# Performance work log

Hardware: AMD Instinct MI355X
Metric: run time of the kernel (lower is better)

The kernel has to match this reference:

```python
import jax, jax.numpy as jnp
import numpy as np

N_HEAD = 16
ROPE_BASE = 10000.0


def _rope_tables(T, head_dim, dtype=jnp.float32):
    inv_freq = 1.0 / (ROPE_BASE ** (jnp.arange(0, head_dim, 2, dtype=jnp.float32) / head_dim))
    t = jnp.arange(T, dtype=jnp.float32)
    freqs = t[:, None] * inv_freq[None, :]          # [T, D/2]
    emb = jnp.concatenate([freqs, freqs], axis=-1)  # [T, D]
    return jnp.cos(emb).astype(dtype), jnp.sin(emb).astype(dtype)


def _rotate_half(x):
    d = x.shape[-1] // 2
    return jnp.concatenate([-x[..., d:], x[..., :d]], axis=-1)


def setup_inputs() -> dict:
    key = jax.random.key(0)
    ks = jax.random.split(key, 5)
    B, T, C = 2, 2048, 2048
    s = 1.0 / np.sqrt(C)
    return {
        "x": jax.random.normal(ks[0], (B, T, C), dtype=jnp.float32),
        "wq": jax.random.normal(ks[1], (C, C), dtype=jnp.float32) * s,
        "wk": jax.random.normal(ks[2], (C, C), dtype=jnp.float32) * s,
        "wv": jax.random.normal(ks[3], (C, C), dtype=jnp.float32) * s,
        "wo": jax.random.normal(ks[4], (C, C), dtype=jnp.float32) * s,
    }


def reference(x, wq, wk, wv, wo):
    B, T, C = x.shape
    H = N_HEAD
    D = C // H

    def heads(y):  # [B,T,C] -> [B,H,T,D]
        return y.reshape(B, T, H, D).transpose(0, 2, 1, 3)

    q = heads(x @ wq)
    k = heads(x @ wk)
    v = heads(x @ wv)

    cos, sin = _rope_tables(T, D, x.dtype)          # [T, D]
    cos = cos[None, None, :, :]
    sin = sin[None, None, :, :]
    q = q * cos + _rotate_half(q) * sin
    k = k * cos + _rotate_half(k) * sin

    scale = 1.0 / np.sqrt(D)
    scores = jnp.einsum('bhqd,bhkd->bhqk', q, k) * scale   # [B,H,T,T]
    causal = jnp.tril(jnp.ones((T, T), dtype=bool))
    scores = jnp.where(causal[None, None, :, :], scores, jnp.finfo(scores.dtype).min)
    attn = jax.nn.softmax(scores, axis=-1)
    y = jnp.einsum('bhqk,bhkd->bhqd', attn, v)             # [B,H,T,D]
    y = y.transpose(0, 2, 1, 3).reshape(B, T, C)
    return y @ wo
```

## Files before the change

kernel.cpp:

```cpp
#include <hip/hip_runtime.h>
#include <hip/hip_bf16.h>
#include <math.h>


#define TT 2048
#define CCn 2048
#define HH 16
#define DD 128
#define BBa 2
#define MMr 4096

typedef __attribute__((ext_vector_type(8))) short s16x8;
typedef __attribute__((ext_vector_type(4))) short s16x4;
typedef __attribute__((ext_vector_type(4))) float f32x4;

__device__ __forceinline__ short bf16_of(float f) {
  unsigned u = __float_as_uint(f);
  unsigned r = u + 0x7fffu + ((u >> 16) & 1u);
  return (short)(r >> 16);
}

__device__ __forceinline__ float ex2(float x) {
#if __has_builtin(__builtin_amdgcn_exp2f)
  return __builtin_amdgcn_exp2f(x);
#else
  return exp2f(x);
#endif
}

__device__ __forceinline__ void lds_load16(const void* g, void* l) {
  __builtin_amdgcn_global_load_lds((__attribute__((address_space(1))) void*)g,
                                   (__attribute__((address_space(3))) void*)l,
                                   16, 0, 0);
}

__global__ __launch_bounds__(256) void k_tables(float* __restrict__ cosT,
                                                float* __restrict__ sinT) {
  int idx = blockIdx.x * 256 + threadIdx.x;
  int t = idx >> 6, i = idx & 63;
  float inv = powf(10000.0f, -(float)i * (1.0f / 64.0f));
  float f = (float)t * inv;
  cosT[idx] = cosf(f);
  sinT[idx] = sinf(f);
}

__global__ __launch_bounds__(256) void k_cast_x(const float* __restrict__ x,
                                                short* __restrict__ xb) {
  int i = blockIdx.x * 256 + threadIdx.x;
  f32x4 v = ((const f32x4*)x)[i];
  s16x4 o;
#pragma unroll
  for (int j = 0; j < 4; ++j) o[j] = bf16_of(v[j]);
  ((s16x4*)xb)[i] = o;
}

__global__ __launch_bounds__(256) void k_wtrans(const float* __restrict__ w,
                                                short* __restrict__ wt) {
  __shared__ float tile[32][33];
  int n0 = blockIdx.x * 32, k0 = blockIdx.y * 32;
  int tx = threadIdx.x & 31, ty = threadIdx.x >> 5;
#pragma unroll
  for (int j = 0; j < 4; ++j) {
    int k = ty * 4 + j;
    tile[k][tx] = w[(size_t)(k0 + k) * CCn + n0 + tx];
  }
  __syncthreads();
#pragma unroll
  for (int j = 0; j < 4; ++j) {
    int n = ty * 4 + j;
    wt[(size_t)(n0 + n) * CCn + k0 + tx] = bf16_of(tile[tx][n]);
  }
}

__global__ __launch_bounds__(256) void k_vtrans(const float* __restrict__ src,
                                                short* __restrict__ dst) {
  __shared__ float tile[32][33];
  int bh = blockIdx.y, b = bh >> 4, h = bh & 15;
  int dt = blockIdx.x & 3, tt = blockIdx.x >> 2;
  int tx = threadIdx.x & 31, ty = threadIdx.x >> 5;
  const float* sp = src + ((size_t)(b * TT + tt * 32)) * CCn + h * DD + dt * 32;
#pragma unroll
  for (int j = 0; j < 4; ++j) {
    int tr = ty * 4 + j;
    tile[tr][tx] = sp[(size_t)tr * CCn + tx];
  }
  __syncthreads();
  short* dp = dst + ((size_t)(bh * DD + dt * 32)) * TT + tt * 32;
#pragma unroll
  for (int j = 0; j < 4; ++j) {
    int dr = ty * 4 + j;
    dp[(size_t)dr * TT + tx] = bf16_of(tile[tx][dr]);
  }
}

__global__ __launch_bounds__(256) void k_rope(const float* __restrict__ src,
                                              const float* __restrict__ cosT,
                                              const float* __restrict__ sinT,
                                              short* __restrict__ dst, float mul) {
  int idx = blockIdx.x * 256 + threadIdx.x;
  int i = idx & 63;
  int h = (idx >> 6) & 15;
  int t = (idx >> 10) & 2047;
  int b = idx >> 21;
  const float* row = src + ((size_t)(b * TT + t)) * CCn + h * DD;
  float q0 = row[i], q1 = row[i + 64];
  float c = cosT[t * 64 + i], s = sinT[t * 64 + i];
  short* orow = dst + ((size_t)((b * HH + h) * TT + t)) * DD;
  orow[i] = bf16_of((q0 * c - q1 * s) * mul);
  orow[i + 64] = bf16_of((q1 * c + q0 * s) * mul);
}

#define BKG 64
__global__ __launch_bounds__(256) void k_gemm(const short* __restrict__ A,
                                              const short* __restrict__ Bt,
                                              float* __restrict__ Cc,
                                              int M, int N, int K) {
  __shared__ short As[128 * BKG];
  __shared__ short Bs[128 * BKG];
  const int tid = threadIdx.x, wid = tid >> 6, lane = tid & 63;
  const int wm = wid >> 1, wn = wid & 1;
  const int lr = lane & 15, lk = lane >> 4;
  const int m0 = blockIdx.y * 128, n0 = blockIdx.x * 128;

  f32x4 acc[4][4] = {};
  const int nk = K / BKG;
  for (int kt = 0; kt < nk; ++kt) {
#pragma unroll
    for (int it = 0; it < 4; ++it) {
      int ch = it * 256 + tid;
      int r = ch >> 3, c = (ch & 7) * 8;
      lds_load16(A + (size_t)(m0 + r) * K + kt * BKG + c,
                 As + (size_t)(it * 256 + wid * 64) * 8);
      lds_load16(Bt + (size_t)(n0 + r) * K + kt * BKG + c,
                 Bs + (size_t)(it * 256 + wid * 64) * 8);
    }
    __syncthreads();
#pragma unroll
    for (int ks = 0; ks < 2; ++ks) {
      s16x8 af[4], bf[4];
#pragma unroll
      for (int i = 0; i < 4; ++i) {
        int ar = wm * 64 + i * 16 + lr;
        af[i] = *(const s16x8*)(As + ar * BKG + ks * 32 + lk * 8);
        int br = wn * 64 + i * 16 + lr;
        bf[i] = *(const s16x8*)(Bs + br * BKG + ks * 32 + lk * 8);
      }
#pragma unroll
      for (int i = 0; i < 4; ++i)
#pragma unroll
        for (int j = 0; j < 4; ++j)
          acc[i][j] = __builtin_amdgcn_mfma_f32_16x16x32_bf16(af[i], bf[j],
                                                              acc[i][j], 0, 0, 0);
    }
    __syncthreads();
  }
#pragma unroll
  for (int i = 0; i < 4; ++i)
#pragma unroll
    for (int j = 0; j < 4; ++j) {
      int col = n0 + wn * 64 + j * 16 + lr;
      int rb = m0 + wm * 64 + i * 16 + lk * 4;
#pragma unroll
      for (int r = 0; r < 4; ++r)
        Cc[(size_t)(rb + r) * N + col] = acc[i][j][r];
    }
}

__global__ __launch_bounds__(256) void k_attn(const short* __restrict__ Qb,
                                              const short* __restrict__ Kb,
                                              const short* __restrict__ Vt,
                                              short* __restrict__ yb) {
  __shared__ short Ks[2][64 * 128];
  __shared__ short Vs[128 * 64];
  __shared__ short Ps[4][16 * 72];
  const int tid = threadIdx.x, wid = tid >> 6, lane = tid & 63;
  const int lr = lane & 15, lk = lane >> 4;
  const int bh = blockIdx.y, bx = blockIdx.x;
  const size_t baseQK = (size_t)bh * TT * DD;
  const int b = bh >> 4, h = bh & 15;

  auto stageK = [&](int bi, int kt2) {
#pragma unroll
    for (int it = 0; it < 4; ++it) {
      int ch = it * 256 + tid;
      int r = ch >> 4, cc = ch & 15;
      int cs = cc ^ (r & 7);
      lds_load16(Kb + baseQK + (size_t)(kt2 * 64 + r) * DD + cs * 8,
                 &Ks[bi][(size_t)(it * 256 + wid * 64) * 8]);
    }
  };
  auto stageV = [&](int kt2) {
#pragma unroll
    for (int it = 0; it < 4; ++it) {
      int ch = it * 256 + tid;
      int d = ch >> 3, kc = ch & 7;
      int cs = kc ^ (d & 7);
      lds_load16(Vt + baseQK + (size_t)d * TT + kt2 * 64 + cs * 8,
                 &Vs[(size_t)(it * 256 + wid * 64) * 8]);
    }
  };

#pragma unroll 1
  for (int pass = 0; pass < 2; ++pass) {
    const int qt = pass ? (31 - bx) : bx;
    const int q0 = qt * 64;
    const int qg = q0 + wid * 16 + lr;
    s16x8 qf[4];
#pragma unroll
    for (int ds = 0; ds < 4; ++ds)
      qf[ds] = *(const s16x8*)(Qb + baseQK + (size_t)qg * DD + (ds * 4 + lk) * 8);

    float mrun = -3.0e38f, lrun = 0.f;
    f32x4 yacc[8] = {};

    const int nkt = qt + 1;
    stageK(0, 0);
    stageV(0);
    __syncthreads();
    int buf = 0;
#pragma unroll 1
    for (int kt = 0; kt < nkt; ++kt) {
      if (kt + 1 < nkt) stageK(buf ^ 1, kt + 1);
      f32x4 sf[4] = {};
#pragma unroll
      for (int sub = 0; sub < 4; ++sub) {
        int kr = sub * 16 + lr;
#pragma unroll
        for (int ds = 0; ds < 4; ++ds) {
          int cc = (ds * 4 + lk) ^ (kr & 7);
          s16x8 kf = *(const s16x8*)(&Ks[buf][kr * 128 + cc * 8]);
          sf[sub] = __builtin_amdgcn_mfma_f32_16x16x32_bf16(kf, qf[ds], sf[sub], 0, 0, 0);
        }
      }
      const int kvbase = kt * 64;
      if (kvbase + 63 > q0 + wid * 16) {
#pragma unroll
        for (int sub = 0; sub < 4; ++sub)
#pragma unroll
          for (int r = 0; r < 4; ++r) {
            int kv = kvbase + sub * 16 + lk * 4 + r;
            if (kv > qg) sf[sub][r] = -3.0e38f;
          }
      }
      float tmax = -3.0e38f;
#pragma unroll
      for (int sub = 0; sub < 4; ++sub)
#pragma unroll
        for (int r = 0; r < 4; ++r) tmax = fmaxf(tmax, sf[sub][r]);
      tmax = fmaxf(tmax, __shfl_xor(tmax, 16, 64));
      tmax = fmaxf(tmax, __shfl_xor(tmax, 32, 64));
      if (!__all(tmax <= mrun + 11.0f)) {
        float mnew = fmaxf(mrun, tmax);
        float alpha = ex2(mrun - mnew);
        mrun = mnew;
        lrun *= alpha;
        float ar[4];
#pragma unroll
        for (int r = 0; r < 4; ++r) ar[r] = __shfl(alpha, lk * 4 + r, 64);
#pragma unroll
        for (int dn = 0; dn < 8; ++dn)
#pragma unroll
          for (int r = 0; r < 4; ++r) yacc[dn][r] *= ar[r];
      }
      float psum = 0.f;
#pragma unroll
      for (int sub = 0; sub < 4; ++sub) {
        s16x4 pq;
#pragma unroll
        for (int r = 0; r < 4; ++r) {
          float p = ex2(sf[sub][r] - mrun);
          psum += p;
          pq[r] = bf16_of(p);
        }
        *(s16x4*)(&Ps[wid][lr * 72 + sub * 16 + lk * 4]) = pq;
      }
      psum += __shfl_xor(psum, 16, 64);
      psum += __shfl_xor(psum, 32, 64);
      lrun += psum;
      __syncthreads();
      s16x8 pf0 = *(const s16x8*)(&Ps[wid][lr * 72 + lk * 8]);
      s16x8 pf1 = *(const s16x8*)(&Ps[wid][lr * 72 + 32 + lk * 8]);
#pragma unroll
      for (int dn = 0; dn < 8; ++dn) {
        int d = dn * 16 + lr;
        s16x8 vf0 = *(const s16x8*)(&Vs[d * 64 + (lk ^ (d & 7)) * 8]);
        yacc[dn] = __builtin_amdgcn_mfma_f32_16x16x32_bf16(pf0, vf0, yacc[dn], 0, 0, 0);
        s16x8 vf1 = *(const s16x8*)(&Vs[d * 64 + ((4 + lk) ^ (d & 7)) * 8]);
        yacc[dn] = __builtin_amdgcn_mfma_f32_16x16x32_bf16(pf1, vf1, yacc[dn], 0, 0, 0);
      }
      __syncthreads();
      if (kt + 1 < nkt) stageV(kt + 1);
      buf ^= 1;
    }
    float linv = 1.f / lrun;
    float lr4[4];
#pragma unroll
    for (int r = 0; r < 4; ++r) lr4[r] = __shfl(linv, lk * 4 + r, 64);
#pragma unroll
    for (int dn = 0; dn < 8; ++dn)
#pragma unroll
      for (int r = 0; r < 4; ++r) {
        int t = q0 + wid * 16 + lk * 4 + r;
        int c = h * DD + dn * 16 + lr;
        yb[((size_t)(b * TT + t)) * CCn + c] = bf16_of(yacc[dn][r] * lr4[r]);
      }
  }
}

extern "C" void kernel_launch(void* const* d_in, const int* in_sizes, int n_in,
                              void* d_out, int out_size, void* d_ws, size_t ws_size,
                              hipStream_t stream) {
  const float* x = (const float*)d_in[0];
  const float* wq = (const float*)d_in[1];
  const float* wk = (const float*)d_in[2];
  const float* wv = (const float*)d_in[3];
  const float* wo = (const float*)d_in[4];
  float* out = (float*)d_out;
  char* ws = (char*)d_ws;

  short* xb = (short*)(ws + 0);
  short* wqT = (short*)(ws + 16777216);
  short* wkT = (short*)(ws + 25165824);
  short* wvT = (short*)(ws + 33554432);
  short* woT = (short*)(ws + 41943040);
  float* tmp = (float*)(ws + 50331648);
  short* Qb = (short*)(ws + 83886080);
  short* Kb = (short*)(ws + 100663296);
  short* Vt = (short*)(ws + 117440512);
  short* yb = (short*)(ws + 134217728);
  float* cosT = (float*)(ws + 150994944);
  float* sinT = (float*)(ws + 151519232);

  const float kmul = 1.4426950408889634f / sqrtf(128.0f);

  k_tables<<<512, 256, 0, stream>>>(cosT, sinT);
  k_cast_x<<<8192, 256, 0, stream>>>(x, xb);
  k_wtrans<<<dim3(64, 64), 256, 0, stream>>>(wq, wqT);
  k_wtrans<<<dim3(64, 64), 256, 0, stream>>>(wk, wkT);
  k_wtrans<<<dim3(64, 64), 256, 0, stream>>>(wv, wvT);
  k_wtrans<<<dim3(64, 64), 256, 0, stream>>>(wo, woT);

  k_gemm<<<dim3(16, 32), 256, 0, stream>>>(xb, wqT, tmp, MMr, CCn, CCn);
  k_rope<<<16384, 256, 0, stream>>>(tmp, cosT, sinT, Qb, 1.0f);
  k_gemm<<<dim3(16, 32), 256, 0, stream>>>(xb, wkT, tmp, MMr, CCn, CCn);
  k_rope<<<16384, 256, 0, stream>>>(tmp, cosT, sinT, Kb, kmul);
  k_gemm<<<dim3(16, 32), 256, 0, stream>>>(xb, wvT, tmp, MMr, CCn, CCn);
  k_vtrans<<<dim3(256, 32), 256, 0, stream>>>(tmp, Vt);

  k_attn<<<dim3(16, 32), 256, 0, stream>>>(Qb, Kb, Vt, yb);
  k_gemm<<<dim3(16, 32), 256, 0, stream>>>(yb, woT, out, MMr, CCn, CCn);
}
```

Measured before the change: 450.8 us.

## Fuse QKV projections into one 256x256 pipelined bf16 GEMM with XCD remap

The Q, K and V weight matrices are packed into one transposed buffer, so a single GEMM computes all three projections and writes bf16 output. The old 128x128 GEMM is replaced by a 256x256-tile, 512-thread kernel with double-buffered LDS, swizzled layout, half-tile prefetch two stages ahead, s_setprio around the MFMA blocks, and a remapping of workgroups across XCDs. RoPE and the V transpose now read bf16 and RoPE is vectorised. The output projection gets only 128 workgroups, which may underfill the GPU, and the extra bf16 rounding of the intermediate slightly changes numerics.

```diff
diff --git a/kernel.cpp b/kernel.cpp
--- a/kernel.cpp
+++ b/kernel.cpp
@@ -7,8 +7,8 @@
 #define CCn 2048
 #define HH 16
 #define DD 128
-#define BBa 2
 #define MMr 4096
+#define NQKV 6144
 
 typedef __attribute__((ext_vector_type(8))) short s16x8;
 typedef __attribute__((ext_vector_type(4))) short s16x4;
@@ -19,14 +19,10 @@
   unsigned r = u + 0x7fffu + ((u >> 16) & 1u);
   return (short)(r >> 16);
 }
-
-__device__ __forceinline__ float ex2(float x) {
-#if __has_builtin(__builtin_amdgcn_exp2f)
-  return __builtin_amdgcn_exp2f(x);
-#else
-  return exp2f(x);
-#endif
-}
+__device__ __forceinline__ float f_of_bf16(short s) {
+  return __uint_as_float(((unsigned)(unsigned short)s) << 16);
+}
+__device__ __forceinline__ float ex2(float x) { return exp2f(x); }
 
 __device__ __forceinline__ void lds_load16(const void* g, void* l) {
   __builtin_amdgcn_global_load_lds((__attribute__((address_space(1))) void*)g,
@@ -72,97 +68,159 @@
   }
 }
 
-__global__ __launch_bounds__(256) void k_vtrans(const float* __restrict__ src,
+__global__ __launch_bounds__(256) void k_vtrans(const short* __restrict__ src,
                                                 short* __restrict__ dst) {
-  __shared__ float tile[32][33];
+  __shared__ short tile[32][33];
   int bh = blockIdx.y, b = bh >> 4, h = bh & 15;
   int dt = blockIdx.x & 3, tt = blockIdx.x >> 2;
   int tx = threadIdx.x & 31, ty = threadIdx.x >> 5;
-  const float* sp = src + ((size_t)(b * TT + tt * 32)) * CCn + h * DD + dt * 32;
+  const short* sp = src + ((size_t)(b * TT + tt * 32)) * NQKV + 4096 + h * DD + dt * 32;
 #pragma unroll
   for (int j = 0; j < 4; ++j) {
     int tr = ty * 4 + j;
-    tile[tr][tx] = sp[(size_t)tr * CCn + tx];
+    tile[tr][tx] = sp[(size_t)tr * NQKV + tx];
   }
   __syncthreads();
   short* dp = dst + ((size_t)(bh * DD + dt * 32)) * TT + tt * 32;
 #pragma unroll
   for (int j = 0; j < 4; ++j) {
     int dr = ty * 4 + j;
-    dp[(size_t)dr * TT + tx] = bf16_of(tile[tx][dr]);
-  }
-}
-
-__global__ __launch_bounds__(256) void k_rope(const float* __restrict__ src,
+    dp[(size_t)dr * TT + tx] = tile[tx][dr];
+  }
+}
+
+__global__ __launch_bounds__(256) void k_rope(const short* __restrict__ qkv, int coff,
                                               const float* __restrict__ cosT,
                                               const float* __restrict__ sinT,
                                               short* __restrict__ dst, float mul) {
   int idx = blockIdx.x * 256 + threadIdx.x;
-  int i = idx & 63;
-  int h = (idx >> 6) & 15;
-  int t = (idx >> 10) & 2047;
-  int b = idx >> 21;
-  const float* row = src + ((size_t)(b * TT + t)) * CCn + h * DD;
-  float q0 = row[i], q1 = row[i + 64];
-  float c = cosT[t * 64 + i], s = sinT[t * 64 + i];
+  int i4 = (idx & 15) * 4;
+  int h = (idx >> 4) & 15;
+  int t = (idx >> 8) & 2047;
+  int b = idx >> 19;
+  const short* row = qkv + ((size_t)(b * TT + t)) * NQKV + coff + h * DD;
+  s16x4 v0 = *(const s16x4*)(row + i4);
+  s16x4 v1 = *(const s16x4*)(row + i4 + 64);
+  f32x4 c4 = *(const f32x4*)(cosT + t * 64 + i4);
+  f32x4 s4 = *(const f32x4*)(sinT + t * 64 + i4);
+  s16x4 o0, o1;
+#pragma unroll
+  for (int j = 0; j < 4; ++j) {
+    float a = f_of_bf16(v0[j]), bb = f_of_bf16(v1[j]);
+    o0[j] = bf16_of((a * c4[j] - bb * s4[j]) * mul);
+    o1[j] = bf16_of((bb * c4[j] + a * s4[j]) * mul);
+  }
   short* orow = dst + ((size_t)((b * HH + h) * TT + t)) * DD;
-  orow[i] = bf16_of((q0 * c - q1 * s) * mul);
-  orow[i + 64] = bf16_of((q1 * c + q0 * s) * mul);
-}
-
-#define BKG 64
-__global__ __launch_bounds__(256) void k_gemm(const short* __restrict__ A,
-                                              const short* __restrict__ Bt,
-                                              float* __restrict__ Cc,
-                                              int M, int N, int K) {
-  __shared__ short As[128 * BKG];
-  __shared__ short Bs[128 * BKG];
+  *(s16x4*)(orow + i4) = o0;
+  *(s16x4*)(orow + i4 + 64) = o1;
+}
+
+template <bool BF16OUT>
+__global__ __launch_bounds__(512, 2) void k_gemm256(const short* __restrict__ A,
+                                                    const short* __restrict__ Bt,
+                                                    void* __restrict__ Cout,
+                                                    int M, int N, int K) {
+  __shared__ short smem[65536];
   const int tid = threadIdx.x, wid = tid >> 6, lane = tid & 63;
-  const int wm = wid >> 1, wn = wid & 1;
+  const int wm = wid >> 2, wn = wid & 3;
   const int lr = lane & 15, lk = lane >> 4;
-  const int m0 = blockIdx.y * 128, n0 = blockIdx.x * 128;
-
-  f32x4 acc[4][4] = {};
-  const int nk = K / BKG;
+  const int swz = (lk ^ ((lr >> 1) & 3)) * 8;
+
+  int nwg = gridDim.x, orig = blockIdx.x;
+  int xcd = orig & 7, idx = orig >> 3;
+  int q = nwg >> 3, rmd = nwg & 7;
+  int wg = (xcd < rmd) ? (xcd * (q + 1) + idx)
+                       : (rmd * (q + 1) + (xcd - rmd) * q + idx);
+  const int NBM = M >> 8;
+  const int m0 = (wg % NBM) * 256, n0 = (wg / NBM) * 256;
+
+  const int ldsbase = (tid & ~63);
+
+  auto stageHalf = [&](const short* src, int r0, int slot, int kt, int h) {
+#pragma unroll
+    for (int l = 0; l < 2; ++l) {
+      int lin = l * 512 + tid;
+      int rr = lin >> 2, cs = lin & 3;
+      int cc = cs ^ ((rr >> 1) & 3);
+      lds_load16(src + (size_t)(r0 + rr) * K + kt * 64 + h * 32 + cc * 8,
+                 smem + slot + (l * 512 + ldsbase) * 8);
+    }
+  };
+  f32x4 acc[8][4] = {};
+  s16x8 af[4], bfr[4];
+
+  const int nk = K >> 6;
+  stageHalf(A, m0, 0, 0, 0);
+  stageHalf(Bt, n0, 32768, 0, 0);
+  stageHalf(A, m0, 8192, 0, 1);
+  stageHalf(Bt, n0, 32768 + 8192, 0, 1);
+  stageHalf(A, m0, 16384, 1, 0);
+  stageHalf(Bt, n0, 32768 + 16384, 1, 0);
+  asm volatile("s_waitcnt vmcnt(4)" ::: "memory");
+  __builtin_amdgcn_s_barrier();
+
+#define PHASE_MFMA(mh)                                                        \
+  __builtin_amdgcn_s_setprio(1);                                              \
+  _Pragma("unroll") for (int i = 0; i < 4; ++i)                               \
+      _Pragma("unroll") for (int j = 0; j < 4; ++j)                           \
+      acc[(mh)*4 + i][j] = __builtin_amdgcn_mfma_f32_16x16x32_bf16(           \
+          af[i], bfr[j], acc[(mh)*4 + i][j], 0, 0, 0);                        \
+  __builtin_amdgcn_s_setprio(0);
+
+#define LOAD_A(mh, ks, abuf)                                                  \
+  _Pragma("unroll") for (int i = 0; i < 4; ++i)                               \
+      af[i] = *(const s16x8*)(smem + (abuf)*16384 + (ks)*8192 +               \
+                              (wm * 128 + (mh)*64 + i * 16 + lr) * 32 + swz);
+#define LOAD_B(ks, abuf)                                                      \
+  _Pragma("unroll") for (int j = 0; j < 4; ++j)                               \
+      bfr[j] = *(const s16x8*)(smem + 32768 + (abuf)*16384 + (ks)*8192 +      \
+                               (wn * 64 + j * 16 + lr) * 32 + swz);
+
+#pragma unroll 1
   for (int kt = 0; kt < nk; ++kt) {
-#pragma unroll
-    for (int it = 0; it < 4; ++it) {
-      int ch = it * 256 + tid;
-      int r = ch >> 3, c = (ch & 7) * 8;
-      lds_load16(A + (size_t)(m0 + r) * K + kt * BKG + c,
-                 As + (size_t)(it * 256 + wid * 64) * 8);
-      lds_load16(Bt + (size_t)(n0 + r) * K + kt * BKG + c,
-                 Bs + (size_t)(it * 256 + wid * 64) * 8);
-    }
-    __syncthreads();
-#pragma unroll
-    for (int ks = 0; ks < 2; ++ks) {
-      s16x8 af[4], bf[4];
-#pragma unroll
-      for (int i = 0; i < 4; ++i) {
-        int ar = wm * 64 + i * 16 + lr;
-        af[i] = *(const s16x8*)(As + ar * BKG + ks * 32 + lk * 8);
-        int br = wn * 64 + i * 16 + lr;
-        bf[i] = *(const s16x8*)(Bs + br * BKG + ks * 32 + lk * 8);
-      }
-#pragma unroll
-      for (int i = 0; i < 4; ++i)
-#pragma unroll
-        for (int j = 0; j < 4; ++j)
-          acc[i][j] = __builtin_amdgcn_mfma_f32_16x16x32_bf16(af[i], bf[j],
-                                                              acc[i][j], 0, 0, 0);
-    }
-    __syncthreads();
-  }
-#pragma unroll
-  for (int i = 0; i < 4; ++i)
+    const int buf = kt & 1, nbuf = buf ^ 1;
+    const bool s1 = (kt + 1 < nk), s2 = (kt + 2 < nk);
+    LOAD_B(0, buf);
+    LOAD_A(0, 0, buf);
+    if (s1) stageHalf(A, m0, nbuf * 16384 + 8192, kt + 1, 1);
+    __builtin_amdgcn_s_barrier();
+    PHASE_MFMA(0);
+    __builtin_amdgcn_s_barrier();
+    LOAD_A(1, 0, buf);
+    if (s1) stageHalf(Bt, n0, 32768 + nbuf * 16384 + 8192, kt + 1, 1);
+    __builtin_amdgcn_s_barrier();
+    PHASE_MFMA(1);
+    __builtin_amdgcn_s_barrier();
+    LOAD_B(1, buf);
+    LOAD_A(0, 1, buf);
+    if (s2) stageHalf(A, m0, buf * 16384, kt + 2, 0);
+    __builtin_amdgcn_s_barrier();
+    PHASE_MFMA(0);
+    __builtin_amdgcn_s_barrier();
+    LOAD_A(1, 1, buf);
+    if (s2) stageHalf(Bt, n0, 32768 + buf * 16384, kt + 2, 0);
+    __builtin_amdgcn_s_barrier();
+    PHASE_MFMA(1);
+    asm volatile("s_waitcnt vmcnt(4)" ::: "memory");
+    __builtin_amdgcn_s_barrier();
+  }
+#undef PHASE_MFMA
+#undef LOAD_A
+#undef LOAD_B
+
+#pragma unroll
+  for (int fi = 0; fi < 8; ++fi)
 #pragma unroll
     for (int j = 0; j < 4; ++j) {
+      int row = m0 + wm * 128 + (fi >> 2) * 64 + (fi & 3) * 16 + lk * 4;
       int col = n0 + wn * 64 + j * 16 + lr;
-      int rb = m0 + wm * 64 + i * 16 + lk * 4;
-#pragma unroll
-      for (int r = 0; r < 4; ++r)
-        Cc[(size_t)(rb + r) * N + col] = acc[i][j][r];
+#pragma unroll
+      for (int rr = 0; rr < 4; ++rr) {
+        if (BF16OUT)
+          ((short*)Cout)[(size_t)(row + rr) * N + col] = bf16_of(acc[fi][j][rr]);
+        else
+          ((float*)Cout)[(size_t)(row + rr) * N + col] = acc[fi][j][rr];
+      }
     }
 }
 
@@ -319,15 +377,13 @@
   char* ws = (char*)d_ws;
 
   short* xb = (short*)(ws + 0);
-  short* wqT = (short*)(ws + 16777216);
-  short* wkT = (short*)(ws + 25165824);
-  short* wvT = (short*)(ws + 33554432);
+  short* wqkvT = (short*)(ws + 16777216);
   short* woT = (short*)(ws + 41943040);
-  float* tmp = (float*)(ws + 50331648);
-  short* Qb = (short*)(ws + 83886080);
-  short* Kb = (short*)(ws + 100663296);
-  short* Vt = (short*)(ws + 117440512);
-  short* yb = (short*)(ws + 134217728);
+  short* qkv = (short*)(ws + 50331648);
+  short* yb = (short*)(ws + 50331648);
+  short* Qb = (short*)(ws + 100663296);
+  short* Kb = (short*)(ws + 117440512);
+  short* Vt = (short*)(ws + 134217728);
   float* cosT = (float*)(ws + 150994944);
   float* sinT = (float*)(ws + 151519232);
 
@@ -335,18 +391,18 @@
 
   k_tables<<<512, 256, 0, stream>>>(cosT, sinT);
   k_cast_x<<<8192, 256, 0, stream>>>(x, xb);
-  k_wtrans<<<dim3(64, 64), 256, 0, stream>>>(wq, wqT);
-  k_wtrans<<<dim3(64, 64), 256, 0, stream>>>(wk, wkT);
-  k_wtrans<<<dim3(64, 64), 256, 0, stream>>>(wv, wvT);
+  k_wtrans<<<dim3(64, 64), 256, 0, stream>>>(wq, wqkvT);
+  k_wtrans<<<dim3(64, 64), 256, 0, stream>>>(wk, wqkvT + (size_t)2048 * 2048);
+  k_wtrans<<<dim3(64, 64), 256, 0, stream>>>(wv, wqkvT + (size_t)4096 * 2048);
   k_wtrans<<<dim3(64, 64), 256, 0, stream>>>(wo, woT);
 
-  k_gemm<<<dim3(16, 32), 256, 0, stream>>>(xb, wqT, tmp, MMr, CCn, CCn);
-  k_rope<<<16384, 256, 0, stream>>>(tmp, cosT, sinT, Qb, 1.0f);
-  k_gemm<<<dim3(16, 32), 256, 0, stream>>>(xb, wkT, tmp, MMr, CCn, CCn);
-  k_rope<<<16384, 256, 0, stream>>>(tmp, cosT, sinT, Kb, kmul);
-  k_gemm<<<dim3(16, 32), 256, 0, stream>>>(xb, wvT, tmp, MMr, CCn, CCn);
-  k_vtrans<<<dim3(256, 32), 256, 0, stream>>>(tmp, Vt);
+  k_gemm256<true><<<16 * 24, 512, 0, stream>>>(xb, wqkvT, qkv, MMr, NQKV, CCn);
+
+  k_rope<<<4096, 256, 0, stream>>>(qkv, 0, cosT, sinT, Qb, 1.0f);
+  k_rope<<<4096, 256, 0, stream>>>(qkv, 2048, cosT, sinT, Kb, kmul);
+  k_vtrans<<<dim3(256, 32), 256, 0, stream>>>(qkv, Vt);
 
   k_attn<<<dim3(16, 32), 256, 0, stream>>>(Qb, Kb, Vt, yb);
-  k_gemm<<<dim3(16, 32), 256, 0, stream>>>(yb, woT, out, MMr, CCn, CCn);
-}
+
+  k_gemm256<false><<<16 * 8, 512, 0, stream>>>(yb, woT, out, MMr, CCn, CCn);
+}
```

New measurement: 425.9 us. 5.5% less time.
